# Kernel tuning notes

Measured on AMD Instinct MI355X. Metric: run time of the kernel, lower is better.

The kernel has to match this reference:

```python
import jax, jax.numpy as jnp
import numpy as np

TEMPERATURE = 0.5
EPS = 1e-12  # matches torch F.normalize default eps


def _l2_normalize(x):
    norm = jnp.sqrt(jnp.sum(x * x, axis=1, keepdims=True))
    return x / jnp.maximum(norm, EPS)


def setup_inputs() -> dict:
    key = jax.random.key(0)
    k1, k2 = jax.random.split(key)
    proj_1 = jax.random.normal(k1, (4096, 128), dtype=jnp.float32)
    proj_2 = jax.random.normal(k2, (4096, 128), dtype=jnp.float32)
    return {"proj_1": proj_1, "proj_2": proj_2}


def reference(proj_1, proj_2):
    batch_size = proj_1.shape[0]
    z_i = _l2_normalize(proj_1)
    z_j = _l2_normalize(proj_2)
    reps = jnp.concatenate([z_i, z_j], axis=0)  # [2B, D], rows unit-norm
    # cosine similarity of unit-norm rows == dot product -> single matmul
    sim = reps @ reps.T  # [2B, 2B]
    # positives: diag offset +B and -B
    pos_ij = jnp.diagonal(sim, offset=batch_size)   # [B]
    pos_ji = jnp.diagonal(sim, offset=-batch_size)  # [B]
    positives = jnp.concatenate([pos_ij, pos_ji], axis=0)  # [2B]
    nominator = jnp.exp(positives / TEMPERATURE)
    n = 2 * batch_size
    mask = 1.0 - jnp.eye(n, dtype=sim.dtype)
    denominator = jnp.sum(mask * jnp.exp(sim / TEMPERATURE), axis=1)  # [2B]
    all_losses = -jnp.log(nominator / denominator)
    return jnp.sum(all_losses) / n
```

## Files before the change

kernel.cpp:

```cpp
#include <hip/hip_runtime.h>
#include <stdint.h>


#define TEMP 0.5f
#define EXP2_SCALE 2.885390081777927f

typedef __bf16 bf16_t;
typedef bf16_t bf16x8 __attribute__((ext_vector_type(8)));
typedef float floatx4 __attribute__((ext_vector_type(4)));

typedef __attribute__((address_space(3))) uint32_t lds_u32;
typedef const __attribute__((address_space(1))) uint32_t glb_u32;

__device__ __forceinline__ unsigned short f32_to_bf16(float f) {
    union { float f; uint32_t u; } v; v.f = f;
    uint32_t u = v.u;
    uint32_t r = (u + 0x7FFFu + ((u >> 16) & 1u)) >> 16;
    return (unsigned short)r;
}

__device__ __forceinline__ bf16x8 as_bf16x8(uint4 v) {
    union { uint4 u; bf16x8 b; } c; c.u = v; return c.b;
}

__device__ __forceinline__ float exp2_raw(float x) {
#if __has_builtin(__builtin_amdgcn_exp2f)
    return __builtin_amdgcn_exp2f(x);
#else
    float r; asm("v_exp_f32 %0, %1" : "=v"(r) : "v"(x)); return r;
#endif
}
__device__ __forceinline__ float log2_raw(float x) {
#if __has_builtin(__builtin_amdgcn_logf)
    return __builtin_amdgcn_logf(x);
#else
    float r; asm("v_log_f32 %0, %1" : "=v"(r) : "v"(x)); return r;
#endif
}

__global__ __launch_bounds__(256) void norm_pos_kernel(
        const float* __restrict__ p1, const float* __restrict__ p2,
        unsigned short* __restrict__ reps, float* __restrict__ pos,
        float* __restrict__ out, int B) {
    if (blockIdx.x == 0 && threadIdx.x == 0) out[0] = 0.f;

    const int slot = threadIdx.x >> 5;
    const int h    = threadIdx.x & 31;
    const int i = blockIdx.x * 8 + slot;
    if (i >= B) return;

    float4 a = ((const float4*)(p1 + (size_t)i * 128))[h];
    float4 b = ((const float4*)(p2 + (size_t)i * 128))[h];
    float ss1 = a.x*a.x + a.y*a.y + a.z*a.z + a.w*a.w;
    float ss2 = b.x*b.x + b.y*b.y + b.z*b.z + b.w*b.w;
    float d   = a.x*b.x + a.y*b.y + a.z*b.z + a.w*b.w;
    #pragma unroll
    for (int off = 16; off > 0; off >>= 1) {
        ss1 += __shfl_xor(ss1, off);
        ss2 += __shfl_xor(ss2, off);
        d   += __shfl_xor(d,   off);
    }
    float rn1 = rsqrtf(fmaxf(ss1, 1e-24f));
    float rn2 = rsqrtf(fmaxf(ss2, 1e-24f));

    ((ushort4*)reps)[(size_t)i * 32 + h] = make_ushort4(
        f32_to_bf16(a.x*rn1), f32_to_bf16(a.y*rn1),
        f32_to_bf16(a.z*rn1), f32_to_bf16(a.w*rn1));
    ((ushort4*)reps)[(size_t)(B + i) * 32 + h] = make_ushort4(
        f32_to_bf16(b.x*rn2), f32_to_bf16(b.y*rn2),
        f32_to_bf16(b.z*rn2), f32_to_bf16(b.w*rn2));

    if (h == 0) pos[i] = d * rn1 * rn2;
}

__global__ __launch_bounds__(256) void simexp_kernel(
        const unsigned short* __restrict__ reps,
        float* __restrict__ part, int nt, int N2) {
    const int tid  = threadIdx.x;
    const int wave = tid >> 6;
    const int lane = tid & 63;
    const int quad = lane >> 4;
    const int l16  = lane & 15;

    int rem = (int)blockIdx.x;
    int by = 0;
    while (rem >= nt - by) { rem -= nt - by; ++by; }
    const int bx = by + rem;
    const bool diag = (bx == by);

    const int rowWave = by * 128 + wave * 32;
    const int colBase = bx * 128;

    const uint4* g4 = (const uint4*)reps;

    __shared__ __align__(16) unsigned short bbuf[8][2048];
    __shared__ float lds_row[128];
    __shared__ float lds_cs[4][128];

    #pragma unroll
    for (int ct = 0; ct < 8; ++ct) {
        const unsigned short* src = reps
            + (size_t)(colBase + ct * 16 + l16) * 128 + wave * 32 + quad * 8;
        __builtin_amdgcn_global_load_lds(
            (glb_u32*)src, (lds_u32*)&bbuf[ct][tid * 8], 16, 0, 0);
    }

    bf16x8 a[2][4];
    #pragma unroll
    for (int tt = 0; tt < 2; ++tt)
        #pragma unroll
        for (int ks = 0; ks < 4; ++ks)
            a[tt][ks] = as_bf16x8(
                g4[(size_t)(rowWave + tt * 16 + l16) * 16 + ks * 4 + quad]);

    float rs[2][4];
    #pragma unroll
    for (int tt = 0; tt < 2; ++tt)
        #pragma unroll
        for (int r = 0; r < 4; ++r) rs[tt][r] = 0.f;

    __syncthreads();

    #pragma unroll
    for (int ct = 0; ct < 8; ++ct) {
        bf16x8 b[4];
        #pragma unroll
        for (int ks = 0; ks < 4; ++ks)
            b[ks] = *(const bf16x8*)&bbuf[ct][ks * 512 + lane * 8];

        floatx4 acc[2];
        acc[0] = (floatx4){0.f, 0.f, 0.f, 0.f};
        acc[1] = (floatx4){0.f, 0.f, 0.f, 0.f};
        #pragma unroll
        for (int ks = 0; ks < 4; ++ks) {
            acc[0] = __builtin_amdgcn_mfma_f32_16x16x32_bf16(a[0][ks], b[ks], acc[0], 0, 0, 0);
            acc[1] = __builtin_amdgcn_mfma_f32_16x16x32_bf16(a[1][ks], b[ks], acc[1], 0, 0, 0);
        }

        if (!diag) {
            float cs = 0.f;
            #pragma unroll
            for (int tt = 0; tt < 2; ++tt)
                #pragma unroll
                for (int r = 0; r < 4; ++r) {
                    float e = exp2_raw(acc[tt][r] * EXP2_SCALE);
                    rs[tt][r] += e;
                    cs += e;
                }
            cs += __shfl_xor(cs, 16);
            cs += __shfl_xor(cs, 32);
            if (lane < 16) lds_cs[wave][ct * 16 + lane] = cs;
        } else {
            const int c = colBase + ct * 16 + l16;
            #pragma unroll
            for (int tt = 0; tt < 2; ++tt) {
                const int rb = rowWave + tt * 16 + quad * 4;
                #pragma unroll
                for (int r = 0; r < 4; ++r) {
                    float e = (rb + r == c) ? 0.f
                             : exp2_raw(acc[tt][r] * EXP2_SCALE);
                    rs[tt][r] += e;
                }
            }
        }
    }

    #pragma unroll
    for (int off = 1; off < 16; off <<= 1)
        #pragma unroll
        for (int tt = 0; tt < 2; ++tt)
            #pragma unroll
            for (int r = 0; r < 4; ++r)
                rs[tt][r] += __shfl_xor(rs[tt][r], off);

    if (l16 == 0) {
        #pragma unroll
        for (int tt = 0; tt < 2; ++tt)
            #pragma unroll
            for (int r = 0; r < 4; ++r)
                lds_row[wave * 32 + tt * 16 + quad * 4 + r] = rs[tt][r];
    }

    __syncthreads();

    if (tid < 128) {
        part[(size_t)bx * N2 + by * 128 + tid] = lds_row[tid];
        if (!diag)
            part[(size_t)by * N2 + colBase + tid] =
                lds_cs[0][tid] + lds_cs[1][tid] + lds_cs[2][tid] + lds_cs[3][tid];
    }
}

__global__ __launch_bounds__(256) void finalize_kernel(
        const float* __restrict__ part, const float* __restrict__ pos,
        float* __restrict__ out, int N2, int B, int nt) {
    const int r = blockIdx.x * 256 + threadIdx.x;
    float s = 0.f;
    #pragma unroll 8
    for (int k = 0; k < nt; ++k) s += part[(size_t)k * N2 + r];

    float local = log2_raw(s) * (0.6931471805599453f / (float)N2);
    if (r < B) local -= pos[r] * (1.0f / ((float)B * TEMP));

    #pragma unroll
    for (int off = 32; off > 0; off >>= 1) local += __shfl_xor(local, off);

    __shared__ float wsum[4];
    const int wave = threadIdx.x >> 6, lane = threadIdx.x & 63;
    if (lane == 0) wsum[wave] = local;
    __syncthreads();
    if (threadIdx.x == 0)
        atomicAdd(out, wsum[0] + wsum[1] + wsum[2] + wsum[3]);
}

extern "C" void kernel_launch(void* const* d_in, const int* in_sizes, int n_in,
                              void* d_out, int out_size, void* d_ws, size_t ws_size,
                              hipStream_t stream) {
    const float* p1 = (const float*)d_in[0];
    const float* p2 = (const float*)d_in[1];
    float* out = (float*)d_out;

    const int B  = in_sizes[0] / 128;
    const int N2 = 2 * B;
    const int nt = N2 / 128;
    const int nb = nt * (nt + 1) / 2;

    unsigned short* reps = (unsigned short*)d_ws;
    float* part = (float*)((char*)d_ws + (size_t)N2 * 256);
    float* pos  = part + (size_t)nt * N2;

    norm_pos_kernel<<<dim3((B + 7) / 8), dim3(256), 0, stream>>>(
        p1, p2, reps, pos, out, B);

    simexp_kernel<<<dim3(nb), dim3(256), 0, stream>>>(reps, part, nt, N2);

    finalize_kernel<<<dim3(N2 / 256), dim3(256), 0, stream>>>(
        part, pos, out, N2, B, nt);
}
```

Before: 85.83 us.

## Make simexp kernel persistent with double-buffered LDS prefetch of next tile

Turns the similarity/exp kernel into a persistent grid of up to 512 blocks, each looping over upper-triangular tiles with a stride. The next tile's B operand is staged into a second LDS buffer and its A fragment is loaded into registers while the current tile computes. The deferred column-sum write is overlapped with the next iteration. The aim is to hide global load latency and cut launch and tail overhead, at the cost of doubled LDS and extra registers, which may lower occupancy.

```diff
diff --git a/kernel.cpp b/kernel.cpp
--- a/kernel.cpp
+++ b/kernel.cpp
@@ -75,120 +75,161 @@
 
 __global__ __launch_bounds__(256) void simexp_kernel(
         const unsigned short* __restrict__ reps,
-        float* __restrict__ part, int nt, int N2) {
+        float* __restrict__ part, int nt, int N2, int nb, int G) {
     const int tid  = threadIdx.x;
     const int wave = tid >> 6;
     const int lane = tid & 63;
     const int quad = lane >> 4;
     const int l16  = lane & 15;
 
-    int rem = (int)blockIdx.x;
-    int by = 0;
+    __shared__ __align__(16) unsigned short bbuf[2][8][2048];
+    __shared__ float lds_cs[2][4][128];
+
+    const uint4* g4 = (const uint4*)reps;
+
+    auto stage = [&](int c, int colBase) {
+        #pragma unroll
+        for (int ct = 0; ct < 8; ++ct) {
+            const unsigned short* src = reps
+                + (size_t)(colBase + ct * 16 + l16) * 128 + wave * 32 + quad * 8;
+            __builtin_amdgcn_global_load_lds(
+                (glb_u32*)src, (lds_u32*)&bbuf[c][ct][tid * 8], 16, 0, 0);
+        }
+    };
+
+    int t = (int)blockIdx.x;
+    if (t >= nb) return;
+    int rem = t, by = 0;
     while (rem >= nt - by) { rem -= nt - by; ++by; }
-    const int bx = by + rem;
-    const bool diag = (bx == by);
-
-    const int rowWave = by * 128 + wave * 32;
-    const int colBase = bx * 128;
-
-    const uint4* g4 = (const uint4*)reps;
-
-    __shared__ __align__(16) unsigned short bbuf[8][2048];
-    __shared__ float lds_row[128];
-    __shared__ float lds_cs[4][128];
-
-    #pragma unroll
-    for (int ct = 0; ct < 8; ++ct) {
-        const unsigned short* src = reps
-            + (size_t)(colBase + ct * 16 + l16) * 128 + wave * 32 + quad * 8;
-        __builtin_amdgcn_global_load_lds(
-            (glb_u32*)src, (lds_u32*)&bbuf[ct][tid * 8], 16, 0, 0);
-    }
-
-    bf16x8 a[2][4];
+    int bx = by + rem;
+
+    bf16x8 aC[2][4], aN[2][4];
     #pragma unroll
     for (int tt = 0; tt < 2; ++tt)
         #pragma unroll
         for (int ks = 0; ks < 4; ++ks)
-            a[tt][ks] = as_bf16x8(
-                g4[(size_t)(rowWave + tt * 16 + l16) * 16 + ks * 4 + quad]);
-
-    float rs[2][4];
-    #pragma unroll
-    for (int tt = 0; tt < 2; ++tt)
-        #pragma unroll
-        for (int r = 0; r < 4; ++r) rs[tt][r] = 0.f;
+            aC[tt][ks] = as_bf16x8(
+                g4[(size_t)(by * 128 + wave * 32 + tt * 16 + l16) * 16 + ks * 4 + quad]);
+    stage(0, bx * 128);
+
+    int cur = 0;
+    int prev_by = 0, prev_bx = 0;
+    bool prev_off = false;
 
     __syncthreads();
 
-    #pragma unroll
-    for (int ct = 0; ct < 8; ++ct) {
-        bf16x8 b[4];
-        #pragma unroll
-        for (int ks = 0; ks < 4; ++ks)
-            b[ks] = *(const bf16x8*)&bbuf[ct][ks * 512 + lane * 8];
-
-        floatx4 acc[2];
-        acc[0] = (floatx4){0.f, 0.f, 0.f, 0.f};
-        acc[1] = (floatx4){0.f, 0.f, 0.f, 0.f};
-        #pragma unroll
-        for (int ks = 0; ks < 4; ++ks) {
-            acc[0] = __builtin_amdgcn_mfma_f32_16x16x32_bf16(a[0][ks], b[ks], acc[0], 0, 0, 0);
-            acc[1] = __builtin_amdgcn_mfma_f32_16x16x32_bf16(a[1][ks], b[ks], acc[1], 0, 0, 0);
-        }
-
-        if (!diag) {
-            float cs = 0.f;
+    while (true) {
+        const int nxt_t = t + G;
+        const bool hasNext = nxt_t < nb;
+        int nby = 0, nbx = 0;
+        if (hasNext) {
+            int r2 = nxt_t;
+            while (r2 >= nt - nby) { r2 -= nt - nby; ++nby; }
+            nbx = nby + r2;
+            stage(cur ^ 1, nbx * 128);
             #pragma unroll
             for (int tt = 0; tt < 2; ++tt)
                 #pragma unroll
-                for (int r = 0; r < 4; ++r) {
-                    float e = exp2_raw(acc[tt][r] * EXP2_SCALE);
-                    rs[tt][r] += e;
-                    cs += e;
-                }
-            cs += __shfl_xor(cs, 16);
-            cs += __shfl_xor(cs, 32);
-            if (lane < 16) lds_cs[wave][ct * 16 + lane] = cs;
-        } else {
-            const int c = colBase + ct * 16 + l16;
-            #pragma unroll
-            for (int tt = 0; tt < 2; ++tt) {
-                const int rb = rowWave + tt * 16 + quad * 4;
-                #pragma unroll
-                for (int r = 0; r < 4; ++r) {
-                    float e = (rb + r == c) ? 0.f
-                             : exp2_raw(acc[tt][r] * EXP2_SCALE);
-                    rs[tt][r] += e;
+                for (int ks = 0; ks < 4; ++ks)
+                    aN[tt][ks] = as_bf16x8(
+                        g4[(size_t)(nby * 128 + wave * 32 + tt * 16 + l16) * 16 + ks * 4 + quad]);
+        }
+
+        if (prev_off && tid < 128)
+            part[(size_t)prev_by * N2 + prev_bx * 128 + tid] =
+                lds_cs[cur ^ 1][0][tid] + lds_cs[cur ^ 1][1][tid]
+              + lds_cs[cur ^ 1][2][tid] + lds_cs[cur ^ 1][3][tid];
+
+        const bool diag = (bx == by);
+        const int colBase = bx * 128;
+        const int rowWave = by * 128 + wave * 32;
+
+        float rs[2][4];
+        #pragma unroll
+        for (int tt = 0; tt < 2; ++tt)
+            #pragma unroll
+            for (int r = 0; r < 4; ++r) rs[tt][r] = 0.f;
+
+        #pragma unroll
+        for (int ct = 0; ct < 8; ++ct) {
+            bf16x8 b[4];
+            #pragma unroll
+            for (int ks = 0; ks < 4; ++ks)
+                b[ks] = *(const bf16x8*)&bbuf[cur][ct][ks * 512 + lane * 8];
+
+            floatx4 acc[2];
+            acc[0] = (floatx4){0.f, 0.f, 0.f, 0.f};
+            acc[1] = (floatx4){0.f, 0.f, 0.f, 0.f};
+            #pragma unroll
+            for (int ks = 0; ks < 4; ++ks) {
+                acc[0] = __builtin_amdgcn_mfma_f32_16x16x32_bf16(aC[0][ks], b[ks], acc[0], 0, 0, 0);
+                acc[1] = __builtin_amdgcn_mfma_f32_16x16x32_bf16(aC[1][ks], b[ks], acc[1], 0, 0, 0);
+            }
+
+            if (!diag) {
+                float cs = 0.f;
+                #pragma unroll
+                for (int tt = 0; tt < 2; ++tt)
+                    #pragma unroll
+                    for (int r = 0; r < 4; ++r) {
+                        float e = exp2_raw(acc[tt][r] * EXP2_SCALE);
+                        rs[tt][r] += e;
+                        cs += e;
+                    }
+                cs += __shfl_xor(cs, 16);
+                cs += __shfl_xor(cs, 32);
+                if (lane < 16) lds_cs[cur][wave][ct * 16 + lane] = cs;
+            } else {
+                const int c = colBase + ct * 16 + l16;
+                #pragma unroll
+                for (int tt = 0; tt < 2; ++tt) {
+                    const int rb = rowWave + tt * 16 + quad * 4;
+                    #pragma unroll
+                    for (int r = 0; r < 4; ++r) {
+                        float e = (rb + r == c) ? 0.f
+                                 : exp2_raw(acc[tt][r] * EXP2_SCALE);
+                        rs[tt][r] += e;
+                    }
                 }
             }
         }
+
+        #pragma unroll
+        for (int off = 1; off < 16; off <<= 1)
+            #pragma unroll
+            for (int tt = 0; tt < 2; ++tt)
+                #pragma unroll
+                for (int r = 0; r < 4; ++r)
+                    rs[tt][r] += __shfl_xor(rs[tt][r], off);
+
+        if (l16 == 0) {
+            #pragma unroll
+            for (int tt = 0; tt < 2; ++tt) {
+                float4 v = make_float4(rs[tt][0], rs[tt][1], rs[tt][2], rs[tt][3]);
+                *(float4*)&part[(size_t)bx * N2 + by * 128
+                                + wave * 32 + tt * 16 + quad * 4] = v;
+            }
+        }
+
+        if (hasNext) {
+            #pragma unroll
+            for (int tt = 0; tt < 2; ++tt)
+                #pragma unroll
+                for (int ks = 0; ks < 4; ++ks)
+                    aC[tt][ks] = aN[tt][ks];
+        }
+        prev_by = by; prev_bx = bx; prev_off = !diag;
+
+        __syncthreads();
+        cur ^= 1;
+        if (!hasNext) break;
+        t = nxt_t; by = nby; bx = nbx;
     }
 
-    #pragma unroll
-    for (int off = 1; off < 16; off <<= 1)
-        #pragma unroll
-        for (int tt = 0; tt < 2; ++tt)
-            #pragma unroll
-            for (int r = 0; r < 4; ++r)
-                rs[tt][r] += __shfl_xor(rs[tt][r], off);
-
-    if (l16 == 0) {
-        #pragma unroll
-        for (int tt = 0; tt < 2; ++tt)
-            #pragma unroll
-            for (int r = 0; r < 4; ++r)
-                lds_row[wave * 32 + tt * 16 + quad * 4 + r] = rs[tt][r];
-    }
-
-    __syncthreads();
-
-    if (tid < 128) {
-        part[(size_t)bx * N2 + by * 128 + tid] = lds_row[tid];
-        if (!diag)
-            part[(size_t)by * N2 + colBase + tid] =
-                lds_cs[0][tid] + lds_cs[1][tid] + lds_cs[2][tid] + lds_cs[3][tid];
-    }
+    if (prev_off && tid < 128)
+        part[(size_t)prev_by * N2 + prev_bx * 128 + tid] =
+            lds_cs[cur ^ 1][0][tid] + lds_cs[cur ^ 1][1][tid]
+          + lds_cs[cur ^ 1][2][tid] + lds_cs[cur ^ 1][3][tid];
 }
 
 __global__ __launch_bounds__(256) void finalize_kernel(
@@ -232,7 +273,9 @@
     norm_pos_kernel<<<dim3((B + 7) / 8), dim3(256), 0, stream>>>(
         p1, p2, reps, pos, out, B);
 
-    simexp_kernel<<<dim3(nb), dim3(256), 0, stream>>>(reps, part, nt, N2);
+    int G = 512;
+    if (G > nb) G = nb;
+    simexp_kernel<<<dim3(G), dim3(256), 0, stream>>>(reps, part, nt, N2, nb, G);
 
     finalize_kernel<<<dim3(N2 / 256), dim3(256), 0, stream>>>(
         part, pos, out, N2, B, nt);
```

Measured after the change: 93.14 us. +8.5%, slower.

## Drop LDS epilogue barrier, write per-wave partials directly, remap blocks across XCDs

Applied to the files above, without the earlier changes.

The simexp kernel no longer stages row and column sums in LDS behind a final __syncthreads. Each wave now writes its row sums as float4 stores and its per-wave column sums to a larger partW buffer, and the finalize kernel reduces the four wave partials itself. Block indices are remapped so that consecutive triangle tiles land on the same XCD, which should improve L2 reuse of shared B tiles, and launch_bounds now requests 5 blocks per CU. The cost is a workspace four times larger for column partials and more global reads in finalize.

```diff
diff --git a/kernel.cpp b/kernel.cpp
--- a/kernel.cpp
+++ b/kernel.cpp
@@ -73,17 +73,23 @@
     if (h == 0) pos[i] = d * rn1 * rn2;
 }
 
-__global__ __launch_bounds__(256) void simexp_kernel(
+__global__ __launch_bounds__(256, 5) void simexp_kernel(
         const unsigned short* __restrict__ reps,
-        float* __restrict__ part, int nt, int N2) {
+        float* __restrict__ partR, float* __restrict__ partW,
+        int nt, int N2, int nb) {
     const int tid  = threadIdx.x;
     const int wave = tid >> 6;
     const int lane = tid & 63;
     const int quad = lane >> 4;
     const int l16  = lane & 15;
 
-    int rem = (int)blockIdx.x;
-    int by = 0;
+    {
+    }
+    const int q8 = nb >> 3, r8 = nb & 7;
+    const int xcd = (int)blockIdx.x & 7, idx = (int)blockIdx.x >> 3;
+    int t = (xcd < r8 ? xcd * (q8 + 1) : r8 * (q8 + 1) + (xcd - r8) * q8) + idx;
+
+    int rem = t, by = 0;
     while (rem >= nt - by) { rem -= nt - by; ++by; }
     const int bx = by + rem;
     const bool diag = (bx == by);
@@ -94,8 +100,6 @@
     const uint4* g4 = (const uint4*)reps;
 
     __shared__ __align__(16) unsigned short bbuf[8][2048];
-    __shared__ float lds_row[128];
-    __shared__ float lds_cs[4][128];
 
     #pragma unroll
     for (int ct = 0; ct < 8; ++ct) {
@@ -118,6 +122,9 @@
     for (int tt = 0; tt < 2; ++tt)
         #pragma unroll
         for (int r = 0; r < 4; ++r) rs[tt][r] = 0.f;
+    float csa[8];
+    #pragma unroll
+    for (int ct = 0; ct < 8; ++ct) csa[ct] = 0.f;
 
     __syncthreads();
 
@@ -149,7 +156,7 @@
                 }
             cs += __shfl_xor(cs, 16);
             cs += __shfl_xor(cs, 32);
-            if (lane < 16) lds_cs[wave][ct * 16 + lane] = cs;
+            csa[ct] = cs;
         } else {
             const int c = colBase + ct * 16 + l16;
             #pragma unroll
@@ -175,29 +182,35 @@
 
     if (l16 == 0) {
         #pragma unroll
-        for (int tt = 0; tt < 2; ++tt)
-            #pragma unroll
-            for (int r = 0; r < 4; ++r)
-                lds_row[wave * 32 + tt * 16 + quad * 4 + r] = rs[tt][r];
-    }
-
-    __syncthreads();
-
-    if (tid < 128) {
-        part[(size_t)bx * N2 + by * 128 + tid] = lds_row[tid];
-        if (!diag)
-            part[(size_t)by * N2 + colBase + tid] =
-                lds_cs[0][tid] + lds_cs[1][tid] + lds_cs[2][tid] + lds_cs[3][tid];
+        for (int tt = 0; tt < 2; ++tt) {
+            float4 v = make_float4(rs[tt][0], rs[tt][1], rs[tt][2], rs[tt][3]);
+            *(float4*)&partR[(size_t)bx * N2 + by * 128
+                             + wave * 32 + tt * 16 + quad * 4] = v;
+        }
+    }
+
+    if (!diag && lane < 16) {
+        float* pw = partW + (size_t)(by * 4 + wave) * N2 + colBase;
+        #pragma unroll
+        for (int ct = 0; ct < 8; ++ct)
+            pw[ct * 16 + l16] = csa[ct];
     }
 }
 
 __global__ __launch_bounds__(256) void finalize_kernel(
-        const float* __restrict__ part, const float* __restrict__ pos,
-        float* __restrict__ out, int N2, int B, int nt) {
-    const int r = blockIdx.x * 256 + threadIdx.x;
+        const float* __restrict__ partR, const float* __restrict__ partW,
+        const float* __restrict__ pos, float* __restrict__ out,
+        int N2, int B, int nt) {
+    const int r  = blockIdx.x * 256 + threadIdx.x;
+    const int by = r >> 7;
+
     float s = 0.f;
-    #pragma unroll 8
-    for (int k = 0; k < nt; ++k) s += part[(size_t)k * N2 + r];
+    for (int k = by; k < nt; ++k) s += partR[(size_t)k * N2 + r];
+    for (int k = 0; k < by; ++k) {
+        const float* pw = partW + (size_t)(k * 4) * N2 + r;
+        s += (pw[0] + pw[(size_t)N2])
+           + (pw[2 * (size_t)N2] + pw[3 * (size_t)N2]);
+    }
 
     float local = log2_raw(s) * (0.6931471805599453f / (float)N2);
     if (r < B) local -= pos[r] * (1.0f / ((float)B * TEMP));
@@ -226,14 +239,16 @@
     const int nb = nt * (nt + 1) / 2;
 
     unsigned short* reps = (unsigned short*)d_ws;
-    float* part = (float*)((char*)d_ws + (size_t)N2 * 256);
-    float* pos  = part + (size_t)nt * N2;
+    float* partR = (float*)((char*)d_ws + (size_t)N2 * 256);
+    float* partW = partR + (size_t)nt * N2;
+    float* pos   = partW + (size_t)nt * 4 * N2;
 
     norm_pos_kernel<<<dim3((B + 7) / 8), dim3(256), 0, stream>>>(
         p1, p2, reps, pos, out, B);
 
-    simexp_kernel<<<dim3(nb), dim3(256), 0, stream>>>(reps, part, nt, N2);
+    simexp_kernel<<<dim3(nb), dim3(256), 0, stream>>>(
+        reps, partR, partW, nt, N2, nb);
 
     finalize_kernel<<<dim3(N2 / 256), dim3(256), 0, stream>>>(
-        part, pos, out, N2, B, nt);
-}
+        partR, partW, pos, out, N2, B, nt);
+}
```

Result: slower. 111.5 us (+29.9%).
